# Kernel optimization log

Hardware: AMD Instinct MI355X
Metric: run time of the kernel (lower is better)

## Reference

```python
import jax, jax.numpy as jnp
import numpy as np

KNN_K = 3
EPS = 1e-8


def _make_poses(key, batch):
    """Random valid SE(3) matrices [B,4,4] (rotation via QR, small translation)."""
    k1, k2 = jax.random.split(key)
    A = jax.random.normal(k1, (batch, 3, 3), dtype=jnp.float32)
    Q, _ = jnp.linalg.qr(A)
    det = jnp.linalg.det(Q)[:, None, None]
    Q = Q * jnp.where(det < 0, -1.0, 1.0)  # ensure proper rotation
    t = jax.random.normal(k2, (batch, 3), dtype=jnp.float32) * 0.5
    pose = jnp.tile(jnp.eye(4, dtype=jnp.float32), (batch, 1, 1))
    pose = pose.at[:, :3, :3].set(Q)
    pose = pose.at[:, :3, 3].set(t)
    return pose


def setup_inputs() -> dict:
    key = jax.random.key(0)
    kq, kr, kf, kp0, kp1 = jax.random.split(key, 5)
    B, N, M = 2, 8192, 8192
    pc0 = jax.random.normal(kq, (B, N, 3), dtype=jnp.float32) * 20.0
    pc1 = jax.random.normal(kr, (B, M, 3), dtype=jnp.float32) * 20.0
    flow1 = jax.random.normal(kf, (B, M, 3), dtype=jnp.float32)
    pose0 = _make_poses(kp0, B)
    pose1 = _make_poses(kp1, B)
    return {"pc0": pc0, "pc1": pc1, "flow1": flow1, "pose0": pose0, "pose1": pose1}


def reference(pc0, pc1, flow1, pose0, pose1):
    # cal_pose0to1: transform from pc0 ego frame into pc1 ego frame
    pose_0to1 = jnp.linalg.inv(pose1) @ pose0            # [B,4,4]
    R = pose_0to1[:, :3, :3]                             # [B,3,3]
    t = pose_0to1[:, :3, 3]                              # [B,3]
    # pc0_in_pc1 = pc0 @ R^T + t
    pc0_t = jnp.einsum("bij,bnj->bni", R, pc0) + t[:, None, :]  # [B,N,3]
    pose_flow = pc0_t - pc0                              # ego-motion displacement

    # pairwise squared distances (cdist^2) via GEMM form: [B,N,M]
    q2 = jnp.sum(pc0_t * pc0_t, axis=-1)                 # [B,N]
    r2 = jnp.sum(pc1 * pc1, axis=-1)                     # [B,M]
    cross = jnp.einsum("bnd,bmd->bnm", pc0_t, pc1)
    d2 = q2[:, :, None] + r2[:, None, :] - 2.0 * cross

    # KNN: k smallest distances
    neg_d2, idx = jax.lax.top_k(-d2, KNN_K)              # [B,N,k]
    d = jnp.sqrt(jnp.maximum(-neg_d2, 0.0))

    # inverse-distance weights over the k neighbors
    w = 1.0 / (d + EPS)
    w = w / jnp.sum(w, axis=-1, keepdims=True)           # [B,N,k]

    # gather neighbor flows: flow1 [B,M,3] -> [B,N,k,3]
    gathered = jnp.take_along_axis(flow1[:, None, :, :], idx[..., None], axis=2)
    flow_interp = jnp.sum(w[..., None] * gathered, axis=2)  # [B,N,3]
    return flow_interp, pose_flow
```

## Files before the change

kernel.cpp:

```cpp
#include <hip/hip_runtime.h>
#include <math.h>
#include <float.h>
#include <limits.h>

#define CS    64
#define CTP   64
#define PASS_PTS (CTP * CS)
#define CSP   65
#define QPB   64
#define QT    8
#define NPASS 2
#define CMSTRIDE 132
#define MARGIN 0.05f
typedef unsigned long long ull;
typedef float v2f __attribute__((ext_vector_type(2)));
#define KMAX 0xFFFFFFFFFFFFFFFFull

__device__ __forceinline__ unsigned int ford(float f) {
    unsigned int b = __float_as_uint(f);
    return b ^ (((unsigned int)((int)b >> 31)) | 0x80000000u);
}
__device__ __forceinline__ float funord(unsigned int u) {
    unsigned int m = ((u >> 31) - 1u) | 0x80000000u;
    return __uint_as_float(u ^ m);
}

__device__ __forceinline__ ull umin64(ull a, ull b) { return a < b ? a : b; }
__device__ __forceinline__ ull umax64(ull a, ull b) { return a > b ? a : b; }

__device__ __forceinline__ void ins3k(ull k, ull& k0, ull& k1, ull& k2) {
    ull n2 = umax64(k1, umin64(k2, k));
    ull n1 = umax64(k0, umin64(k1, k));
    k0 = umin64(k0, k);
    k1 = n1;
    k2 = n2;
}

__device__ __forceinline__ void sins(float d, float& a0, float& a1, float& a2)
{
    float n1 = __builtin_amdgcn_fmed3f(a0, a1, d);
    float n2 = __builtin_amdgcn_fmed3f(a1, a2, d);
    a0 = fminf(a0, d);
    a1 = n1;
    a2 = n2;
}

__device__ __forceinline__ void pose_rel(const float* __restrict__ P0,
                                         const float* __restrict__ P1,
                                         float R[3][3], float tv[3])
{
    float dt0 = P0[3]  - P1[3];
    float dt1 = P0[7]  - P1[7];
    float dt2 = P0[11] - P1[11];
    #pragma unroll
    for (int i = 0; i < 3; ++i) {
        float a0 = P1[i], a1 = P1[4 + i], a2 = P1[8 + i];
        #pragma unroll
        for (int j = 0; j < 3; ++j)
            R[i][j] = fmaf(a2, P0[8 + j], fmaf(a1, P0[4 + j], a0 * P0[j]));
        tv[i] = fmaf(a2, dt2, fmaf(a1, dt1, a0 * dt0));
    }
}

__launch_bounds__(512, 2)
__global__ void knn_fused(const float* __restrict__ pc0,
                          const float* __restrict__ pc1,
                          const float* __restrict__ flow1,
                          const float* __restrict__ pose0,
                          const float* __restrict__ pose1,
                          float* __restrict__ out,
                          int B, int N, int M)
{
    __shared__ float4 tile[CTP * CSP];
    __shared__ float4 qd[QPB];

    const int tid = threadIdx.x;
    const int b   = blockIdx.y;
    const int qb  = blockIdx.x * QPB;

    if (tid < QPB) {
        float R[3][3], tv[3];
        pose_rel(pose0 + b * 16, pose1 + b * 16, R, tv);
        int qg0 = qb + tid;
        bool valid = qg0 < N;
        int qg = valid ? qg0 : (N - 1);
        const float px = pc0[(size_t)(b * N + qg) * 3 + 0];
        const float py = pc0[(size_t)(b * N + qg) * 3 + 1];
        const float pz = pc0[(size_t)(b * N + qg) * 3 + 2];
        float qx = fmaf(R[0][2], pz, fmaf(R[0][1], py, R[0][0] * px)) + tv[0];
        float qy = fmaf(R[1][2], pz, fmaf(R[1][1], py, R[1][0] * px)) + tv[1];
        float qz = fmaf(R[2][2], pz, fmaf(R[2][1], py, R[2][0] * px)) + tv[2];
        qd[tid] = make_float4(qx, qy, qz, (qx * qx + qy * qy) + qz * qz);
        if (valid) {
            size_t pf = (size_t)B * N * 3 + (size_t)(b * N + qg) * 3;
            out[pf + 0] = qx - px;
            out[pf + 1] = qy - py;
            out[pf + 2] = qz - pz;
        }
    }
    __syncthreads();

    const int w    = tid >> 6;
    const int lane = tid & 63;

    v2f qx2[QT], qy2[QT], qz2[QT];
    #pragma unroll
    for (int t = 0; t < QT; ++t) {
        float4 qq = qd[w * QT + t];
        qx2[t] = (v2f)(qq.x);
        qy2[t] = (v2f)(qq.y);
        qz2[t] = (v2f)(qq.z);
    }

    float mm[NPASS][QT];
    #pragma unroll
    for (int pp = 0; pp < NPASS; ++pp)
        #pragma unroll
        for (int t = 0; t < QT; ++t) mm[pp][t] = FLT_MAX;

    for (int pass = 0; pass < NPASS; ++pass) {
        if (pass) __syncthreads();

        #pragma unroll
        for (int k = 0; k < PASS_PTS / (512 * 4); ++k) {
            const int pl = (tid + k * 512) * 4;
            const int p  = pass * PASS_PTS + pl;
            const int c  = pl >> 6;
            const int off = pl & (CS - 1);
            float4* dst = &tile[c * CSP + off];
            float x0,y0,z0, x1,y1,z1, x2,y2,z2, x3,y3,z3;
            if (p + 3 < M) {
                const float4* pf = (const float4*)(pc1 + (size_t)(b * M + p) * 3);
                float4 A = pf[0], Bv = pf[1], C = pf[2];
                x0 = A.x;  y0 = A.y;  z0 = A.z;
                x1 = A.w;  y1 = Bv.x; z1 = Bv.y;
                x2 = Bv.z; y2 = Bv.w; z2 = C.x;
                x3 = C.y;  y3 = C.z;  z3 = C.w;
            } else {
                float tx[4], ty[4], tz[4];
                #pragma unroll
                for (int u = 0; u < 4; ++u) {
                    int pp2 = p + u;
                    if (pp2 < M) {
                        const float* s = pc1 + (size_t)(b * M + pp2) * 3;
                        tx[u] = s[0]; ty[u] = s[1]; tz[u] = s[2];
                    } else {
                        tx[u] = 0.f; ty[u] = 0.f; tz[u] = 0.f;
                    }
                }
                x0 = tx[0]; y0 = ty[0]; z0 = tz[0];
                x1 = tx[1]; y1 = ty[1]; z1 = tz[1];
                x2 = tx[2]; y2 = ty[2]; z2 = tz[2];
                x3 = tx[3]; y3 = ty[3]; z3 = tz[3];
            }
            float r0 = (p + 0 < M) ? (x0 * x0 + y0 * y0) + z0 * z0 : FLT_MAX;
            float r1 = (p + 1 < M) ? (x1 * x1 + y1 * y1) + z1 * z1 : FLT_MAX;
            float r2 = (p + 2 < M) ? (x2 * x2 + y2 * y2) + z2 * z2 : FLT_MAX;
            float r3 = (p + 3 < M) ? (x3 * x3 + y3 * y3) + z3 * z3 : FLT_MAX;
            dst[0] = make_float4(-2.f * x0, -2.f * x1, -2.f * y0, -2.f * y1);
            dst[1] = make_float4(-2.f * z0, -2.f * z1, r0, r1);
            dst[2] = make_float4(-2.f * x2, -2.f * x3, -2.f * y2, -2.f * y3);
            dst[3] = make_float4(-2.f * z2, -2.f * z3, r2, r3);
        }
        __syncthreads();

        const float4* tp = &tile[lane * CSP];
        #pragma unroll 4
        for (int i = 0; i < 32; ++i) {
            const float4 xy = tp[2 * i];
            const float4 zw = tp[2 * i + 1];
            v2f X = {xy.x, xy.y};
            v2f Y = {xy.z, xy.w};
            v2f Z = {zw.x, zw.y};
            v2f W = {zw.z, zw.w};
            #pragma unroll
            for (int t = 0; t < QT; ++t) {
                v2f kk;
                asm("v_pk_fma_f32 %0, %1, %2, %3"
                    : "=v"(kk) : "v"(Z), "v"(qz2[t]), "v"(W));
                asm("v_pk_fma_f32 %0, %1, %2, %0"
                    : "+v"(kk) : "v"(Y), "v"(qy2[t]));
                asm("v_pk_fma_f32 %0, %1, %2, %0"
                    : "+v"(kk) : "v"(X), "v"(qx2[t]));
                mm[pass][t] = fminf(mm[pass][t], fminf(kk.x, kk.y));
            }
        }
    }

    __syncthreads();

    float* cminL = (float*)tile;
    #pragma unroll
    for (int t = 0; t < QT; ++t) {
        const int ql = w * QT + t;
        cminL[ql * CMSTRIDE + lane]       = mm[0][t];
        cminL[ql * CMSTRIDE + CTP + lane] = mm[1][t];
    }
    __syncthreads();

    const int g = tid >> 4;
    const int l = tid & 15;

    for (int round = 0; round < QPB / 32; ++round) {
        const int ql = round * 32 + g;
        const int q0 = qb + ql;
        const bool qvalid = (q0 < N);
        const int q = qvalid ? q0 : (N - 1);

        const float4 sA = *(const float4*)&cminL[ql * CMSTRIDE + l * 8];
        const float4 sB = *(const float4*)&cminL[ql * CMSTRIDE + l * 8 + 4];
        const float4 qq = qd[ql];
        const float qx = qq.x, qy = qq.y, qz = qq.z, q2 = qq.w;

        float a0 = FLT_MAX, a1 = FLT_MAX, a2 = FLT_MAX;
        sins(sA.x, a0, a1, a2); sins(sA.y, a0, a1, a2);
        sins(sA.z, a0, a1, a2); sins(sA.w, a0, a1, a2);
        sins(sB.x, a0, a1, a2); sins(sB.y, a0, a1, a2);
        sins(sB.z, a0, a1, a2); sins(sB.w, a0, a1, a2);
        #pragma unroll
        for (int msk = 1; msk <= 8; msk <<= 1) {
            float o0 = __shfl_xor(a0, msk);
            float o1 = __shfl_xor(a1, msk);
            float o2 = __shfl_xor(a2, msk);
            sins(o0, a0, a1, a2);
            sins(o1, a0, a1, a2);
            sins(o2, a0, a1, a2);
        }
        const float thr = a2 + MARGIN;

        unsigned int mbits =
              ((unsigned int)(sA.x <= thr) << 0) | ((unsigned int)(sA.y <= thr) << 1)
            | ((unsigned int)(sA.z <= thr) << 2) | ((unsigned int)(sA.w <= thr) << 3)
            | ((unsigned int)(sB.x <= thr) << 4) | ((unsigned int)(sB.y <= thr) << 5)
            | ((unsigned int)(sB.z <= thr) << 6) | ((unsigned int)(sB.w <= thr) << 7);
        ull m0 = (l < 8) ? ((ull)mbits << (8 * l)) : 0ull;
        ull m1 = (l >= 8) ? ((ull)mbits << (8 * (l - 8))) : 0ull;
        #pragma unroll
        for (int msk = 1; msk <= 8; msk <<= 1) {
            m0 |= __shfl_xor(m0, msk);
            m1 |= __shfl_xor(m1, msk);
        }

        ull kA0 = KMAX, kA1 = KMAX, kA2 = KMAX;
        ull kB0 = KMAX, kB1 = KMAX, kB2 = KMAX;
        #pragma unroll
        for (int half = 0; half < 2; ++half) {
            ull mask = half ? m1 : m0;
            const int cbase = half * 64;
            while (mask) {
                const int ck = (int)__builtin_ctzll(mask);
                mask &= mask - 1;
                const int mb = (cbase + ck) * CS;
                #pragma unroll
                for (int r = 0; r < CS / 16; ++r) {
                    const int m = mb + r * 16 + l;
                    if (m < M) {
                        const float* pp = pc1 + (size_t)(b * M + m) * 3;
                        float x = pp[0], y = pp[1], z = pp[2];
                        float r2 = (x * x + y * y) + z * z;
                        float cr = fmaf(qz, z, fmaf(qy, y, qx * x));
                        float dd = fmaf(-2.0f, cr, q2 + r2);
                        ull kk = ((ull)ford(dd) << 32) | (unsigned int)m;
                        if (r & 1) ins3k(kk, kB0, kB1, kB2);
                        else       ins3k(kk, kA0, kA1, kA2);
                    }
                }
            }
        }
        ins3k(kB0, kA0, kA1, kA2);
        ins3k(kB1, kA0, kA1, kA2);
        ins3k(kB2, kA0, kA1, kA2);

        #pragma unroll
        for (int msk = 1; msk <= 8; msk <<= 1) {
            ull o0 = __shfl_xor(kA0, msk);
            ull o1 = __shfl_xor(kA1, msk);
            ull o2 = __shfl_xor(kA2, msk);
            ins3k(o0, kA0, kA1, kA2);
            ins3k(o1, kA0, kA1, kA2);
            ins3k(o2, kA0, kA1, kA2);
        }

        if (l == 0 && qvalid) {
            float D0 = funord((unsigned int)(kA0 >> 32));
            float D1 = funord((unsigned int)(kA1 >> 32));
            float D2 = funord((unsigned int)(kA2 >> 32));
            int   i0 = (int)(unsigned int)kA0;
            int   i1 = (int)(unsigned int)kA1;
            int   i2 = (int)(unsigned int)kA2;

            float dd0 = sqrtf(fmaxf(D0, 0.f));
            float dd1 = sqrtf(fmaxf(D1, 0.f));
            float dd2 = sqrtf(fmaxf(D2, 0.f));
            float w0 = 1.0f / (dd0 + 1e-8f);
            float w1 = 1.0f / (dd1 + 1e-8f);
            float w2 = 1.0f / (dd2 + 1e-8f);
            float wsum = (w0 + w1) + w2;
            w0 /= wsum; w1 /= wsum; w2 /= wsum;

            const float* f0 = flow1 + (size_t)(b * M + i0) * 3;
            const float* f1 = flow1 + (size_t)(b * M + i1) * 3;
            const float* f2 = flow1 + (size_t)(b * M + i2) * 3;

            const size_t ob = (size_t)(b * N + q) * 3;
            #pragma unroll
            for (int c = 0; c < 3; ++c) {
                float p0 = w0 * f0[c];
                float p1 = w1 * f1[c];
                float p2 = w2 * f2[c];
                out[ob + c] = (p0 + p1) + p2;
            }
        }
    }
}

extern "C" void kernel_launch(void* const* d_in, const int* in_sizes, int n_in,
                              void* d_out, int out_size, void* d_ws, size_t ws_size,
                              hipStream_t stream) {
    const float* pc0   = (const float*)d_in[0];
    const float* pc1   = (const float*)d_in[1];
    const float* flow1 = (const float*)d_in[2];
    const float* pose0 = (const float*)d_in[3];
    const float* pose1 = (const float*)d_in[4];
    float* out = (float*)d_out;

    const int B = in_sizes[3] / 16;
    const int N = in_sizes[0] / (3 * B);
    const int M = in_sizes[1] / (3 * B);

    dim3 grid((N + QPB - 1) / QPB, B);
    knn_fused<<<grid, dim3(512), 0, stream>>>(pc0, pc1, flow1, pose0, pose1,
                                              out, B, N, M);
}
```

Before: 37.48 us.

## Replace packed-FMA SoA tile with AoS float4 tile and rotated-index bank spreading

```diff
diff --git a/kernel.cpp b/kernel.cpp
--- a/kernel.cpp
+++ b/kernel.cpp
@@ -6,14 +6,12 @@
 #define CS    64
 #define CTP   64
 #define PASS_PTS (CTP * CS)
-#define CSP   65
 #define QPB   64
 #define QT    8
 #define NPASS 2
 #define CMSTRIDE 132
 #define MARGIN 0.05f
 typedef unsigned long long ull;
-typedef float v2f __attribute__((ext_vector_type(2)));
 #define KMAX 0xFFFFFFFFFFFFFFFFull
 
 __device__ __forceinline__ unsigned int ford(float f) {
@@ -71,7 +69,7 @@
                           float* __restrict__ out,
                           int B, int N, int M)
 {
-    __shared__ float4 tile[CTP * CSP];
+    __shared__ float4 tile[PASS_PTS];
     __shared__ float4 qd[QPB];
 
     const int tid = threadIdx.x;
@@ -103,14 +101,9 @@
     const int w    = tid >> 6;
     const int lane = tid & 63;
 
-    v2f qx2[QT], qy2[QT], qz2[QT];
+    float4 qv[QT];
     #pragma unroll
-    for (int t = 0; t < QT; ++t) {
-        float4 qq = qd[w * QT + t];
-        qx2[t] = (v2f)(qq.x);
-        qy2[t] = (v2f)(qq.y);
-        qz2[t] = (v2f)(qq.z);
-    }
+    for (int t = 0; t < QT; ++t) qv[t] = qd[w * QT + t];
 
     float mm[NPASS][QT];
     #pragma unroll
@@ -125,65 +118,45 @@
         for (int k = 0; k < PASS_PTS / (512 * 4); ++k) {
             const int pl = (tid + k * 512) * 4;
             const int p  = pass * PASS_PTS + pl;
-            const int c  = pl >> 6;
-            const int off = pl & (CS - 1);
-            float4* dst = &tile[c * CSP + off];
-            float x0,y0,z0, x1,y1,z1, x2,y2,z2, x3,y3,z3;
+            float4* dst = &tile[pl];
             if (p + 3 < M) {
                 const float4* pf = (const float4*)(pc1 + (size_t)(b * M + p) * 3);
                 float4 A = pf[0], Bv = pf[1], C = pf[2];
-                x0 = A.x;  y0 = A.y;  z0 = A.z;
-                x1 = A.w;  y1 = Bv.x; z1 = Bv.y;
-                x2 = Bv.z; y2 = Bv.w; z2 = C.x;
-                x3 = C.y;  y3 = C.z;  z3 = C.w;
+                dst[0] = make_float4(-2.f * A.x, -2.f * A.y, -2.f * A.z,
+                                     (A.x * A.x + A.y * A.y) + A.z * A.z);
+                dst[1] = make_float4(-2.f * A.w, -2.f * Bv.x, -2.f * Bv.y,
+                                     (A.w * A.w + Bv.x * Bv.x) + Bv.y * Bv.y);
+                dst[2] = make_float4(-2.f * Bv.z, -2.f * Bv.w, -2.f * C.x,
+                                     (Bv.z * Bv.z + Bv.w * Bv.w) + C.x * C.x);
+                dst[3] = make_float4(-2.f * C.y, -2.f * C.z, -2.f * C.w,
+                                     (C.y * C.y + C.z * C.z) + C.w * C.w);
             } else {
-                float tx[4], ty[4], tz[4];
                 #pragma unroll
                 for (int u = 0; u < 4; ++u) {
                     int pp2 = p + u;
+                    float4 v;
                     if (pp2 < M) {
                         const float* s = pc1 + (size_t)(b * M + pp2) * 3;
-                        tx[u] = s[0]; ty[u] = s[1]; tz[u] = s[2];
+                        float x = s[0], y = s[1], z = s[2];
+                        v = make_float4(-2.f * x, -2.f * y, -2.f * z,
+                                        (x * x + y * y) + z * z);
                     } else {
-                        tx[u] = 0.f; ty[u] = 0.f; tz[u] = 0.f;
+                        v = make_float4(0.f, 0.f, 0.f, FLT_MAX);
                     }
+                    dst[u] = v;
                 }
-                x0 = tx[0]; y0 = ty[0]; z0 = tz[0];
-                x1 = tx[1]; y1 = ty[1]; z1 = tz[1];
-                x2 = tx[2]; y2 = ty[2]; z2 = tz[2];
-                x3 = tx[3]; y3 = ty[3]; z3 = tz[3];
             }
-            float r0 = (p + 0 < M) ? (x0 * x0 + y0 * y0) + z0 * z0 : FLT_MAX;
-            float r1 = (p + 1 < M) ? (x1 * x1 + y1 * y1) + z1 * z1 : FLT_MAX;
-            float r2 = (p + 2 < M) ? (x2 * x2 + y2 * y2) + z2 * z2 : FLT_MAX;
-            float r3 = (p + 3 < M) ? (x3 * x3 + y3 * y3) + z3 * z3 : FLT_MAX;
-            dst[0] = make_float4(-2.f * x0, -2.f * x1, -2.f * y0, -2.f * y1);
-            dst[1] = make_float4(-2.f * z0, -2.f * z1, r0, r1);
-            dst[2] = make_float4(-2.f * x2, -2.f * x3, -2.f * y2, -2.f * y3);
-            dst[3] = make_float4(-2.f * z2, -2.f * z3, r2, r3);
         }
         __syncthreads();
 
-        const float4* tp = &tile[lane * CSP];
+        const float4* cb = &tile[lane << 6];
         #pragma unroll 4
-        for (int i = 0; i < 32; ++i) {
-            const float4 xy = tp[2 * i];
-            const float4 zw = tp[2 * i + 1];
-            v2f X = {xy.x, xy.y};
-            v2f Y = {xy.z, xy.w};
-            v2f Z = {zw.x, zw.y};
-            v2f W = {zw.z, zw.w};
+        for (int i = 0; i < CS; ++i) {
+            const float4 v = cb[(i + lane) & (CS - 1)];
             #pragma unroll
-            for (int t = 0; t < QT; ++t) {
-                v2f kk;
-                asm("v_pk_fma_f32 %0, %1, %2, %3"
-                    : "=v"(kk) : "v"(Z), "v"(qz2[t]), "v"(W));
-                asm("v_pk_fma_f32 %0, %1, %2, %0"
-                    : "+v"(kk) : "v"(Y), "v"(qy2[t]));
-                asm("v_pk_fma_f32 %0, %1, %2, %0"
-                    : "+v"(kk) : "v"(X), "v"(qx2[t]));
-                mm[pass][t] = fminf(mm[pass][t], fminf(kk.x, kk.y));
-            }
+            for (int t = 0; t < QT; ++t)
+                mm[pass][t] = fminf(mm[pass][t],
+                    fmaf(qv[t].x, v.x, fmaf(qv[t].y, v.y, fmaf(qv[t].z, v.z, v.w))));
         }
     }
 
```

Result: faster. 34.36 us (-8.3%).
